# Performance work log

Hardware: AMD Instinct MI355X
Metric: run time of the kernel (lower is better)

Reference implementation:

```python
import jax, jax.numpy as jnp
import numpy as np

B, S, E, H = 2, 2048, 1024, 16
D = E // H  # head_dim

def setup_inputs() -> dict:
    key = jax.random.key(0)
    k1, k2, k3 = jax.random.split(key, 3)
    x = jax.random.normal(k1, (B, S, E), dtype=jnp.float32)
    # xavier-uniform-ish scale for the learned projections
    lim_qkv = np.sqrt(6.0 / (E + 3 * E)).astype(np.float32)
    lim_out = np.sqrt(6.0 / (E + E)).astype(np.float32)
    w_qkv = jax.random.uniform(k2, (E, 3 * E), jnp.float32, -lim_qkv, lim_qkv)
    w_out = jax.random.uniform(k3, (E, E), jnp.float32, -lim_out, lim_out)
    return {"x": x, "w_qkv": w_qkv, "w_out": w_out}

def reference(x, w_qkv, w_out):
    b, s, e = x.shape
    # QKV projection: (B,S,E) @ (E,3E) -> (B,S,3E)
    qkv = jnp.einsum('bse,ef->bsf', x, w_qkv)
    qkv = qkv.reshape(b, s, 3, H, D).transpose(2, 0, 3, 1, 4)  # (3,B,H,S,D)
    q, k, v = qkv[0], qkv[1], qkv[2]
    scale = 1.0 / np.sqrt(D).astype(np.float32)
    scores = jnp.einsum('bhsd,bhtd->bhst', q, k) * scale  # (B,H,S,S)
    attn = jax.nn.softmax(scores, axis=-1)
    out = jnp.einsum('bhst,bhtd->bhsd', attn, v)  # (B,H,S,D)
    out = out.transpose(0, 2, 1, 3).reshape(b, s, e)
    return jnp.einsum('bse,ef->bsf', out, w_out)
```

## Files before the change

### kernel.cpp

```cpp
#include <hip/hip_runtime.h>
#include <cstdint>


typedef __bf16 bf16;
typedef __bf16 bf16x4 __attribute__((ext_vector_type(4)));
typedef __bf16 bf16x8 __attribute__((ext_vector_type(8)));
typedef float floatx4 __attribute__((ext_vector_type(4)));
typedef uint32_t u32;

#define B_ 2
#define S_ 2048
#define E_ 1024
#define H_ 16
#define D_ 64

__device__ __forceinline__ void async16(const void* g, const void* l) {
  __builtin_amdgcn_global_load_lds(
      (u32 __attribute__((address_space(1)))*)g,
      (u32 __attribute__((address_space(3)))*)l,
      16, 0, 0);
}

__global__ __launch_bounds__(256) void prep(
    bf16* __restrict__ xt, bf16* __restrict__ wqt, bf16* __restrict__ wot,
    const float* __restrict__ x, const float* __restrict__ wqkv,
    const float* __restrict__ wout) {
  const int id = blockIdx.x;
  const int tid = threadIdx.x;
  if (id < 1024) {
    const bf16 isW = (id < 768);
    const int i2 = isW ? id : id - 768;
    const int nblk = i2 >> 5, t = i2 & 31;
    const float* src = isW ? wqkv : wout;
    bf16* dst = isW ? wqt : wot;
    const int C = isW ? 3072 : 1024;
#pragma unroll
    for (int p = 0; p < 2; ++p) {
      const int u = p * 256 + tid;
      const int kg = u >> 7, row = u & 127;
      const float* s = src + (size_t)(t * 32 + kg * 8) * C + nblk * 128 + row;
      bf16x8 o;
#pragma unroll
      for (int j = 0; j < 8; ++j) o[j] = (bf16)s[(size_t)j * C];
      *(bf16x8*)(dst + ((((size_t)nblk * 32 + t) * 4 + kg) * 128 + row) * 8) = o;
    }
  } else {
    const int i3 = id - 1024;
    const int mblk = i3 >> 5, t = i3 & 31;
#pragma unroll
    for (int p = 0; p < 2; ++p) {
      const int u = p * 256 + tid;
      const int kg = u >> 7, row = u & 127;
      const floatx4* s = (const floatx4*)(
          x + (size_t)(mblk * 128 + row) * 1024 + t * 32 + kg * 8);
      floatx4 v0 = s[0], v1 = s[1];
      bf16x8 o;
#pragma unroll
      for (int j = 0; j < 4; ++j) { o[j] = (bf16)v0[j]; o[4 + j] = (bf16)v1[j]; }
      *(bf16x8*)(xt + ((((size_t)mblk * 32 + t) * 4 + kg) * 128 + row) * 8) = o;
    }
  }
}

__global__ __launch_bounds__(256) void gemm_qkv(
    bf16* __restrict__ qb, bf16* __restrict__ kst, bf16* __restrict__ vst,
    const bf16* __restrict__ At, const bf16* __restrict__ Bt) {
  __shared__ alignas(16) bf16 sA[3][4096];
  __shared__ alignas(16) bf16 sB[3][4096];
  const int tid = threadIdx.x;
  const int lane = tid & 63;
  const int w = tid >> 6;
  const int wr = (w >> 1) * 64, wc = (w & 1) * 64;
  const int l15 = lane & 15, l4 = lane >> 4;
  const int m0 = blockIdx.x * 128;
  const int n0 = blockIdx.y * 128;

  const bf16* ga0 = At + (size_t)blockIdx.x * 131072 + (w * 128 + lane) * 8;
  const bf16* gb0 = Bt + (size_t)blockIdx.y * 131072 + (w * 128 + lane) * 8;
  const int da0 = (w * 128 + lane) * 8;

  floatx4 acc[4][4];
#pragma unroll
  for (int i = 0; i < 4; ++i)
#pragma unroll
    for (int j = 0; j < 4; ++j) acc[i][j] = (floatx4){0.f, 0.f, 0.f, 0.f};

#pragma unroll
  for (int tb = 0; tb < 2; ++tb)
#pragma unroll
    for (int g = 0; g < 2; ++g) {
      async16(ga0 + (size_t)tb * 4096 + g * 512, &sA[tb][da0 + g * 512]);
      async16(gb0 + (size_t)tb * 4096 + g * 512, &sB[tb][da0 + g * 512]);
    }
  asm volatile("s_waitcnt vmcnt(4)" ::: "memory");
  asm volatile("s_barrier" ::: "memory");

  int cur = 0, stb = 2;
  for (int t = 0; t < 32; ++t) {
    if (t < 30) {
      const size_t k0 = (size_t)(t + 2) * 4096;
#pragma unroll
      for (int g = 0; g < 2; ++g) {
        async16(ga0 + k0 + g * 512, &sA[stb][da0 + g * 512]);
        async16(gb0 + k0 + g * 512, &sB[stb][da0 + g * 512]);
      }
    }

    bf16x8 af[4], bfr[4];
#pragma unroll
    for (int i = 0; i < 4; ++i)
      af[i] = *(const bf16x8*)&sA[cur][(l4 * 128 + wr + i * 16 + l15) * 8];
#pragma unroll
    for (int j = 0; j < 4; ++j)
      bfr[j] = *(const bf16x8*)&sB[cur][(l4 * 128 + wc + j * 16 + l15) * 8];

    __builtin_amdgcn_s_setprio(1);
#pragma unroll
    for (int i = 0; i < 4; ++i)
#pragma unroll
      for (int j = 0; j < 4; ++j)
        acc[i][j] = __builtin_amdgcn_mfma_f32_16x16x32_bf16(af[i], bfr[j],
                                                            acc[i][j], 0, 0, 0);
    __builtin_amdgcn_s_setprio(0);

    if (t < 30)
      asm volatile("s_waitcnt vmcnt(4)" ::: "memory");
    else
      asm volatile("s_waitcnt vmcnt(0)" ::: "memory");
    asm volatile("s_barrier" ::: "memory");

    cur = (cur == 2) ? 0 : cur + 1;
    stb = (stb == 2) ? 0 : stb + 1;
  }

  if (n0 < E_) {
#pragma unroll
    for (int i = 0; i < 4; ++i)
#pragma unroll
      for (int j = 0; j < 4; ++j)
#pragma unroll
        for (int r = 0; r < 4; ++r) {
          const int row = m0 + wr + i * 16 + l4 * 4 + r;
          const int col = n0 + wc + j * 16 + l15;
          qb[(size_t)row * E_ + col] = (bf16)acc[i][j][r];
        }
  } else if (n0 < 2 * E_) {
#pragma unroll
    for (int i = 0; i < 4; ++i)
#pragma unroll
      for (int j = 0; j < 4; ++j) {
        const int f = n0 - E_ + wc + j * 16 + l15;
        const int h = f >> 6, d = f & 63;
        const int kg = d >> 3, jd = d & 7;
        const int row0 = m0 + wr + i * 16 + l4 * 4;
        const int b = row0 >> 11, s0 = row0 & 2047;
        const int tt = s0 >> 6, key0 = s0 & 63;
        const size_t base =
            ((((size_t)(b * H_ + h) * 32 + tt) * 8 + kg) * 64 + key0) * 8 + jd;
#pragma unroll
        for (int r = 0; r < 4; ++r)
          kst[base + (size_t)r * 8] = (bf16)acc[i][j][r];
      }
  } else {
#pragma unroll
    for (int i = 0; i < 4; ++i)
#pragma unroll
      for (int j = 0; j < 4; ++j) {
        const int f = n0 - 2 * E_ + wc + j * 16 + l15;
        const int h = f >> 6, d = f & 63;
        const int row0 = m0 + wr + i * 16 + l4 * 4;
        const int b = row0 >> 11, s0 = row0 & 2047;
        const int tt = s0 >> 6, k6 = s0 & 63;
        const int kg = (k6 >> 5) * 4 + ((k6 >> 2) & 3);
        const int e0 = ((k6 >> 4) & 1) * 4;
        bf16x4 o;
#pragma unroll
        for (int r = 0; r < 4; ++r) o[r] = (bf16)acc[i][j][r];
        *(bf16x4*)(vst +
                   ((((size_t)(b * H_ + h) * 32 + tt) * 8 + kg) * 64 + d) * 8 +
                   e0) = o;
      }
  }
}

template <typename OutT>
__global__ __launch_bounds__(256) void gemm_bt64(
    OutT* __restrict__ C, const bf16* __restrict__ At, const bf16* __restrict__ Bt,
    int M, int N, int K) {
  __shared__ alignas(16) bf16 sA[3][2048];
  __shared__ alignas(16) bf16 sB[3][4096];
  const int tid = threadIdx.x;
  const int lane = tid & 63;
  const int w = tid >> 6;
  const int wr = (w >> 1) * 32, wc = (w & 1) * 64;
  const int l15 = lane & 15, l4 = lane >> 4;
  const int m0 = blockIdx.x * 64;
  const int n0 = blockIdx.y * 128;

  const bf16* ga0 = At + (size_t)blockIdx.x * (K * 64) + (w * 64 + lane) * 8;
  const bf16* gb0 = Bt + (size_t)blockIdx.y * (K * 128) + (w * 128 + lane) * 8;
  const int daA = (w * 64 + lane) * 8;
  const int daB = (w * 128 + lane) * 8;

  floatx4 acc[2][4];
#pragma unroll
  for (int i = 0; i < 2; ++i)
#pragma unroll
    for (int j = 0; j < 4; ++j) acc[i][j] = (floatx4){0.f, 0.f, 0.f, 0.f};

#pragma unroll
  for (int tb = 0; tb < 2; ++tb) {
    async16(ga0 + (size_t)tb * 2048, &sA[tb][daA]);
#pragma unroll
    for (int g = 0; g < 2; ++g)
      async16(gb0 + (size_t)tb * 4096 + g * 512, &sB[tb][daB + g * 512]);
  }
  asm volatile("s_waitcnt vmcnt(3)" ::: "memory");
  asm volatile("s_barrier" ::: "memory");

  int cur = 0, stb = 2;
  const int NT = K / 32;
  for (int t = 0; t < NT; ++t) {
    if (t < NT - 2) {
      async16(ga0 + (size_t)(t + 2) * 2048, &sA[stb][daA]);
#pragma unroll
      for (int g = 0; g < 2; ++g)
        async16(gb0 + (size_t)(t + 2) * 4096 + g * 512, &sB[stb][daB + g * 512]);
    }

    bf16x8 af[2], bfr[4];
#pragma unroll
    for (int i = 0; i < 2; ++i)
      af[i] = *(const bf16x8*)&sA[cur][(l4 * 64 + wr + i * 16 + l15) * 8];
#pragma unroll
    for (int j = 0; j < 4; ++j)
      bfr[j] = *(const bf16x8*)&sB[cur][(l4 * 128 + wc + j * 16 + l15) * 8];

    __builtin_amdgcn_s_setprio(1);
#pragma unroll
    for (int i = 0; i < 2; ++i)
#pragma unroll
      for (int j = 0; j < 4; ++j)
        acc[i][j] = __builtin_amdgcn_mfma_f32_16x16x32_bf16(af[i], bfr[j],
                                                            acc[i][j], 0, 0, 0);
    __builtin_amdgcn_s_setprio(0);

    if (t < NT - 2)
      asm volatile("s_waitcnt vmcnt(3)" ::: "memory");
    else
      asm volatile("s_waitcnt vmcnt(0)" ::: "memory");
    asm volatile("s_barrier" ::: "memory");

    cur = (cur == 2) ? 0 : cur + 1;
    stb = (stb == 2) ? 0 : stb + 1;
  }

#pragma unroll
  for (int i = 0; i < 2; ++i)
#pragma unroll
    for (int j = 0; j < 4; ++j)
#pragma unroll
      for (int r = 0; r < 4; ++r) {
        const int row = m0 + wr + i * 16 + l4 * 4 + r;
        const int col = n0 + wc + j * 16 + l15;
        C[(size_t)row * N + col] = (OutT)acc[i][j][r];
      }
}

__global__ __launch_bounds__(256) void attn_flash(
    bf16* __restrict__ at, const bf16* __restrict__ qb,
    const bf16* __restrict__ kst, const bf16* __restrict__ vst) {
  __shared__ alignas(16) bf16 sK[2][4096];
  __shared__ alignas(16) bf16 sV[2][4096];
  const int tid = threadIdx.x;
  const int lane = tid & 63;
  const int w = tid >> 6;
  const int l15 = lane & 15, l4 = lane >> 4;
  const int bh = blockIdx.x;
  const int q0 = blockIdx.y * 64;
  const int b = bh >> 4, h = bh & 15;
  const bf16* kb = kst + (size_t)bh * (S_ * D_);
  const bf16* vb = vst + (size_t)bh * (S_ * D_);

  bf16x8 qf[2];
#pragma unroll
  for (int ks = 0; ks < 2; ++ks) {
    bf16x8 t = *(const bf16x8*)(qb +
        (size_t)(b * S_ + q0 + w * 16 + l15) * E_ + h * D_ + ks * 32 + l4 * 8);
#pragma unroll
    for (int e = 0; e < 8; ++e)
      t[e] = (bf16)((float)t[e] * 0.180336878f);
    qf[ks] = t;
  }

  floatx4 O[4];
#pragma unroll
  for (int j = 0; j < 4; ++j) O[j] = (floatx4){0.f, 0.f, 0.f, 0.f};
  float l_s = 0.f;

#pragma unroll
  for (int j = 0; j < 2; ++j) {
    const int kg = w * 2 + j;
    async16(kb + (size_t)(kg * 64 + lane) * 8, &sK[0][(kg * 64 + lane) * 8]);
    async16(vb + (size_t)(kg * 64 + lane) * 8, &sV[0][(kg * 64 + lane) * 8]);
  }

  for (int t = 0; t < 32; ++t) {
    const int cur = t & 1, nxt = cur ^ 1;
    __syncthreads();

    if (t < 31) {
#pragma unroll
      for (int j = 0; j < 2; ++j) {
        const int kg = w * 2 + j;
        const size_t goff = ((size_t)((t + 1) * 8 + kg) * 64 + lane) * 8;
        async16(kb + goff, &sK[nxt][(kg * 64 + lane) * 8]);
        async16(vb + goff, &sV[nxt][(kg * 64 + lane) * 8]);
      }
    }

    floatx4 sc[4];
#pragma unroll
    for (int j = 0; j < 4; ++j) sc[j] = (floatx4){-16.f, -16.f, -16.f, -16.f};
#pragma unroll
    for (int ks = 0; ks < 2; ++ks) {
      bf16x8 kf[4];
#pragma unroll
      for (int kt = 0; kt < 4; ++kt)
        kf[kt] = *(const bf16x8*)&sK[cur][((ks * 4 + l4) * 64 + kt * 16 + l15) * 8];
#pragma unroll
      for (int kt = 0; kt < 4; ++kt)
        sc[kt] = __builtin_amdgcn_mfma_f32_16x16x32_bf16(
            kf[kt], qf[ks], sc[kt], 0, 0, 0);
    }

    float rs = 0.f;
    bf16x8 pf[2];
#pragma unroll
    for (int kt = 0; kt < 4; ++kt) {
#pragma unroll
      for (int r = 0; r < 4; ++r) {
        const float p = __builtin_amdgcn_exp2f(sc[kt][r]);
        rs += p;
        pf[kt >> 1][(kt & 1) * 4 + r] = (bf16)p;
      }
    }
    l_s += rs;

#pragma unroll
    for (int ks = 0; ks < 2; ++ks) {
      bf16x8 vf[4];
#pragma unroll
      for (int dt = 0; dt < 4; ++dt)
        vf[dt] = *(const bf16x8*)&sV[cur][((ks * 4 + l4) * 64 + dt * 16 + l15) * 8];
#pragma unroll
      for (int dt = 0; dt < 4; ++dt)
        O[dt] = __builtin_amdgcn_mfma_f32_16x16x32_bf16(vf[dt], pf[ks], O[dt], 0, 0, 0);
    }
  }

  float l = l_s;
  l += __shfl_xor(l, 16);
  l += __shfl_xor(l, 32);
  const float inv_l = 1.f / l;
  const int mblk = b * 32 + blockIdx.y;
  const int row6 = w * 16 + l15;
#pragma unroll
  for (int dt = 0; dt < 4; ++dt) {
    bf16x4 o;
#pragma unroll
    for (int r = 0; r < 4; ++r) o[r] = (bf16)(O[dt][r] * inv_l);
    const int tt = h * 2 + (dt >> 1);
    const int kg = (dt & 1) * 2 + (l4 >> 1);
    const int jd = (l4 & 1) * 4;
    *(bf16x4*)(at +
               ((((size_t)mblk * 32 + tt) * 4 + kg) * 64 + row6) * 8 + jd) = o;
  }
}

extern "C" void kernel_launch(void* const* d_in, const int* in_sizes, int n_in,
                              void* d_out, int out_size, void* d_ws, size_t ws_size,
                              hipStream_t stream) {
  const float* x = (const float*)d_in[0];
  const float* wqkv = (const float*)d_in[1];
  const float* wout = (const float*)d_in[2];
  float* out = (float*)d_out;

  bf16* ws = (bf16*)d_ws;
  bf16* xt = ws;
  bf16* qb = xt + (size_t)4096 * 1024;
  bf16* wqt = qb + (size_t)4096 * 1024;
  bf16* wot = wqt + (size_t)3072 * 1024;
  bf16* kst = wot + (size_t)1024 * 1024;
  bf16* vst = kst + (size_t)B_ * H_ * S_ * D_;
  bf16* at = vst + (size_t)B_ * H_ * S_ * D_;

  prep<<<dim3(2048), 256, 0, stream>>>(xt, wqt, wot, x, wqkv, wout);
  gemm_qkv<<<dim3(32, 24), 256, 0, stream>>>(qb, kst, vst, xt, wqt);
  attn_flash<<<dim3(B_ * H_, S_ / 64), 256, 0, stream>>>(at, qb, kst, vst);
  gemm_bt64<float><<<dim3(64, 8), 256, 0, stream>>>(out, at, wot, 4096, E_, E_);
}
```

Measured before the change: 177.7 us.

## Process two query tiles per wave in flash attention to reuse K/V fragments

Each attention block now covers 128 query rows instead of 64, with every wave handling two 16-row query tiles. The K and V fragments loaded from LDS are reused across both tiles, and each staged K/V chunk serves twice as many queries, so LDS reads and global K/V traffic per query are halved. The grid shrinks to 512 blocks and register use per thread roughly doubles for accumulators. The added launch_bounds occupancy hint may constrain register allocation. The softmax still uses a fixed max offset with no running max, as before.

```diff
diff --git a/kernel.cpp b/kernel.cpp
--- a/kernel.cpp
+++ b/kernel.cpp
@@ -267,7 +267,7 @@
       }
 }
 
-__global__ __launch_bounds__(256) void attn_flash(
+__global__ __launch_bounds__(256, 4) void attn_flash(
     bf16* __restrict__ at, const bf16* __restrict__ qb,
     const bf16* __restrict__ kst, const bf16* __restrict__ vst) {
   __shared__ alignas(16) bf16 sK[2][4096];
@@ -277,26 +277,31 @@
   const int w = tid >> 6;
   const int l15 = lane & 15, l4 = lane >> 4;
   const int bh = blockIdx.x;
-  const int q0 = blockIdx.y * 64;
+  const int q0 = blockIdx.y * 128;
   const int b = bh >> 4, h = bh & 15;
   const bf16* kb = kst + (size_t)bh * (S_ * D_);
   const bf16* vb = vst + (size_t)bh * (S_ * D_);
 
-  bf16x8 qf[2];
-#pragma unroll
-  for (int ks = 0; ks < 2; ++ks) {
-    bf16x8 t = *(const bf16x8*)(qb +
-        (size_t)(b * S_ + q0 + w * 16 + l15) * E_ + h * D_ + ks * 32 + l4 * 8);
-#pragma unroll
-    for (int e = 0; e < 8; ++e)
-      t[e] = (bf16)((float)t[e] * 0.180336878f);
-    qf[ks] = t;
-  }
-
-  floatx4 O[4];
-#pragma unroll
-  for (int j = 0; j < 4; ++j) O[j] = (floatx4){0.f, 0.f, 0.f, 0.f};
-  float l_s = 0.f;
+  bf16x8 qf[2][2];
+#pragma unroll
+  for (int qt = 0; qt < 2; ++qt)
+#pragma unroll
+    for (int ks = 0; ks < 2; ++ks) {
+      bf16x8 t = *(const bf16x8*)(qb +
+          (size_t)(b * S_ + q0 + w * 32 + qt * 16 + l15) * E_ +
+          h * D_ + ks * 32 + l4 * 8);
+#pragma unroll
+      for (int e = 0; e < 8; ++e)
+        t[e] = (bf16)((float)t[e] * 0.180336878f);
+      qf[qt][ks] = t;
+    }
+
+  floatx4 O[2][4];
+#pragma unroll
+  for (int qt = 0; qt < 2; ++qt)
+#pragma unroll
+    for (int j = 0; j < 4; ++j) O[qt][j] = (floatx4){0.f, 0.f, 0.f, 0.f};
+  float l_s[2] = {0.f, 0.f};
 
 #pragma unroll
   for (int j = 0; j < 2; ++j) {
@@ -319,9 +324,12 @@
       }
     }
 
-    floatx4 sc[4];
-#pragma unroll
-    for (int j = 0; j < 4; ++j) sc[j] = (floatx4){-16.f, -16.f, -16.f, -16.f};
+    floatx4 sc[2][4];
+#pragma unroll
+    for (int qt = 0; qt < 2; ++qt)
+#pragma unroll
+      for (int j = 0; j < 4; ++j)
+        sc[qt][j] = (floatx4){-16.f, -16.f, -16.f, -16.f};
 #pragma unroll
     for (int ks = 0; ks < 2; ++ks) {
       bf16x8 kf[4];
@@ -329,23 +337,28 @@
       for (int kt = 0; kt < 4; ++kt)
         kf[kt] = *(const bf16x8*)&sK[cur][((ks * 4 + l4) * 64 + kt * 16 + l15) * 8];
 #pragma unroll
-      for (int kt = 0; kt < 4; ++kt)
-        sc[kt] = __builtin_amdgcn_mfma_f32_16x16x32_bf16(
-            kf[kt], qf[ks], sc[kt], 0, 0, 0);
-    }
-
-    float rs = 0.f;
-    bf16x8 pf[2];
-#pragma unroll
-    for (int kt = 0; kt < 4; ++kt) {
-#pragma unroll
-      for (int r = 0; r < 4; ++r) {
-        const float p = __builtin_amdgcn_exp2f(sc[kt][r]);
-        rs += p;
-        pf[kt >> 1][(kt & 1) * 4 + r] = (bf16)p;
-      }
-    }
-    l_s += rs;
+      for (int qt = 0; qt < 2; ++qt)
+#pragma unroll
+        for (int kt = 0; kt < 4; ++kt)
+          sc[qt][kt] = __builtin_amdgcn_mfma_f32_16x16x32_bf16(
+              kf[kt], qf[qt][ks], sc[qt][kt], 0, 0, 0);
+    }
+
+    bf16x8 pf[2][2];
+#pragma unroll
+    for (int qt = 0; qt < 2; ++qt) {
+      float rs = 0.f;
+#pragma unroll
+      for (int kt = 0; kt < 4; ++kt) {
+#pragma unroll
+        for (int r = 0; r < 4; ++r) {
+          const float p = __builtin_amdgcn_exp2f(sc[qt][kt][r]);
+          rs += p;
+          pf[qt][kt >> 1][(kt & 1) * 4 + r] = (bf16)p;
+        }
+      }
+      l_s[qt] += rs;
+    }
 
 #pragma unroll
     for (int ks = 0; ks < 2; ++ks) {
@@ -354,27 +367,33 @@
       for (int dt = 0; dt < 4; ++dt)
         vf[dt] = *(const bf16x8*)&sV[cur][((ks * 4 + l4) * 64 + dt * 16 + l15) * 8];
 #pragma unroll
-      for (int dt = 0; dt < 4; ++dt)
-        O[dt] = __builtin_amdgcn_mfma_f32_16x16x32_bf16(vf[dt], pf[ks], O[dt], 0, 0, 0);
-    }
-  }
-
-  float l = l_s;
-  l += __shfl_xor(l, 16);
-  l += __shfl_xor(l, 32);
-  const float inv_l = 1.f / l;
-  const int mblk = b * 32 + blockIdx.y;
-  const int row6 = w * 16 + l15;
-#pragma unroll
-  for (int dt = 0; dt < 4; ++dt) {
-    bf16x4 o;
-#pragma unroll
-    for (int r = 0; r < 4; ++r) o[r] = (bf16)(O[dt][r] * inv_l);
-    const int tt = h * 2 + (dt >> 1);
-    const int kg = (dt & 1) * 2 + (l4 >> 1);
-    const int jd = (l4 & 1) * 4;
-    *(bf16x4*)(at +
-               ((((size_t)mblk * 32 + tt) * 4 + kg) * 64 + row6) * 8 + jd) = o;
+      for (int qt = 0; qt < 2; ++qt)
+#pragma unroll
+        for (int dt = 0; dt < 4; ++dt)
+          O[qt][dt] = __builtin_amdgcn_mfma_f32_16x16x32_bf16(
+              vf[dt], pf[qt][ks], O[qt][dt], 0, 0, 0);
+    }
+  }
+
+#pragma unroll
+  for (int qt = 0; qt < 2; ++qt) {
+    float l = l_s[qt];
+    l += __shfl_xor(l, 16);
+    l += __shfl_xor(l, 32);
+    const float inv_l = 1.f / l;
+    const int mblk = b * 32 + blockIdx.y * 2 + (w >> 1);
+    const int row6 = (w & 1) * 32 + qt * 16 + l15;
+#pragma unroll
+    for (int dt = 0; dt < 4; ++dt) {
+      bf16x4 o;
+#pragma unroll
+      for (int r = 0; r < 4; ++r) o[r] = (bf16)(O[qt][dt][r] * inv_l);
+      const int tt = h * 2 + (dt >> 1);
+      const int kg = (dt & 1) * 2 + (l4 >> 1);
+      const int jd = (l4 & 1) * 4;
+      *(bf16x4*)(at +
+                 ((((size_t)mblk * 32 + tt) * 4 + kg) * 64 + row6) * 8 + jd) = o;
+    }
   }
 }
 
@@ -397,6 +416,6 @@
 
   prep<<<dim3(2048), 256, 0, stream>>>(xt, wqt, wot, x, wqkv, wout);
   gemm_qkv<<<dim3(32, 24), 256, 0, stream>>>(qb, kst, vst, xt, wqt);
-  attn_flash<<<dim3(B_ * H_, S_ / 64), 256, 0, stream>>>(at, qb, kst, vst);
+  attn_flash<<<dim3(B_ * H_, S_ / 128), 256, 0, stream>>>(at, qb, kst, vst);
   gemm_bt64<float><<<dim3(64, 8), 256, 0, stream>>>(out, at, wot, 4096, E_, E_);
 }
```

After: 179.1 us. No clear change (+0.8%).
